# Optimization experiments

Hardware: AMD Instinct MI355X
Metric: run time of the kernel (lower is better)

The kernel has to match this reference:

```python
import jax, jax.numpy as jnp
import numpy as np

N = 50000      # nodes
E = 800000     # edges
IN = 300       # input feature dim (wiki-cs)
H = 5          # attention heads (hardcoded in module)
D = 32         # hidden dim per head
OUT = 10       # output classes (wiki-cs)
NEG = 0.2      # leaky relu negative slope (hardcoded)


def setup_inputs() -> dict:
    key = jax.random.key(0)
    ks = jax.random.split(key, 18)
    def gl(k, shape, fan_in):
        return jax.random.normal(k, shape, jnp.float32) * (1.0 / np.sqrt(fan_in))
    return {
        "features": jax.random.normal(ks[0], (N, IN), jnp.float32),
        "src": jax.random.randint(ks[1], (E,), 0, N, dtype=jnp.int32),
        "dst": jax.random.randint(ks[2], (E,), 0, N, dtype=jnp.int32),
        "W0": gl(ks[3], (IN, H * D), IN),
        "al0": gl(ks[4], (H, D), D),
        "ar0": gl(ks[5], (H, D), D),
        "W1": gl(ks[6], (H * D, H * D), H * D),
        "al1": gl(ks[7], (H, D), D),
        "ar1": gl(ks[8], (H, D), D),
        "W2": gl(ks[9], (H * D, H * D), H * D),
        "al2": gl(ks[10], (H, D), D),
        "ar2": gl(ks[11], (H, D), D),
        "Wout": gl(ks[12], (H * D, OUT), H * D),
        "alout": gl(ks[13], (1, OUT), OUT),
        "arout": gl(ks[14], (1, OUT), OUT),
        "Wraw": gl(ks[15], (IN, H * D), IN),
        "braw": jnp.zeros((H * D,), jnp.float32),
    }


def _gat(x, W, al, ar, src, dst):
    # DGL GATConv: project, per-edge LeakyReLU attention logits,
    # segment-softmax over incoming edges per dst node, weighted scatter-sum.
    Hh, Dd = al.shape
    feat = (x @ W).reshape(N, Hh, Dd)                 # [N,H,D]
    el = jnp.sum(feat * al, axis=-1)                  # [N,H]
    er = jnp.sum(feat * ar, axis=-1)                  # [N,H]
    e = jax.nn.leaky_relu(el[src] + er[dst], NEG)     # [E,H]
    emax = jax.ops.segment_max(e, dst, num_segments=N)
    ew = jnp.exp(e - emax[dst])
    denom = jax.ops.segment_sum(ew, dst, num_segments=N)
    alpha = ew / denom[dst]                           # [E,H]
    msg = feat[src] * alpha[:, :, None]               # [E,H,D]
    return jax.ops.segment_sum(msg, dst, num_segments=N)  # [N,H,D]


def reference(features, src, dst, W0, al0, ar0, W1, al1, ar1, W2, al2, ar2,
              Wout, alout, arout, Wraw, braw):
    # degree-normalized residual aggregation (GResConv with graph_res=raw_res=True)
    deg = jax.ops.segment_sum(jnp.ones((E,), jnp.float32), dst, num_segments=N)
    norm = jnp.maximum(deg, 1.0) ** -0.5              # [N]
    raw = features @ Wraw + braw                      # [N, H*D]
    # input conv: GAT + relu + flatten
    h = jax.nn.relu(_gat(features, W0, al0, ar0, src, dst)).reshape(N, H * D)
    for (W, al, ar) in ((W1, al1, ar1), (W2, al2, ar2)):
        res = raw * norm[:, None]
        res = jax.ops.segment_sum(res[src], dst, num_segments=N) * norm[:, None]
        h = jax.nn.relu(_gat(h, W, al, ar, src, dst).reshape(N, H * D) + res)
    out = _gat(h, Wout, alout, arout, src, dst)       # [N,1,OUT]
    return out.mean(axis=1)                           # [N,OUT]
```

## Files before the change

### kernel.cpp

```cpp
#include <hip/hip_runtime.h>
#include <hip/hip_bf16.h>

#define NEGS 0.2f

typedef __attribute__((ext_vector_type(8))) short bf16x8;
typedef __attribute__((ext_vector_type(4))) float f32x4;

__device__ inline unsigned short bf16_rne(float x) {
    unsigned u = __float_as_uint(x);
    unsigned r = u + 0x7FFFu + ((u >> 16) & 1u);
    return (unsigned short)(r >> 16);
}

__global__ void k_degi(const int* __restrict__ dst, int* __restrict__ deg, int E) {
    int e = blockIdx.x * blockDim.x + threadIdx.x;
    if (e < E) atomicAdd(&deg[dst[e]], 1);
}

__global__ __launch_bounds__(256)
void k_scan1(const int* __restrict__ deg, int* __restrict__ rowptr,
             int* __restrict__ bsum, float* __restrict__ norm, int N) {
    __shared__ int sdata[256];
    int t = threadIdx.x, i = blockIdx.x * 256 + t;
    int d = (i < N) ? deg[i] : 0;
    sdata[t] = d;
    __syncthreads();
    for (int off = 1; off < 256; off <<= 1) {
        int v = (t >= off) ? sdata[t - off] : 0;
        __syncthreads();
        sdata[t] += v;
        __syncthreads();
    }
    if (i < N) {
        rowptr[i] = sdata[t] - d;
        norm[i] = rsqrtf(fmaxf((float)d, 1.0f));
    }
    if (t == 255) bsum[blockIdx.x] = sdata[255];
}

__global__ __launch_bounds__(256)
void k_scan2(const int* __restrict__ bsum, int* __restrict__ boff,
             int* __restrict__ rowptrN, int nb) {
    __shared__ int sdata[256];
    int t = threadIdx.x;
    int v = (t < nb) ? bsum[t] : 0;
    sdata[t] = v;
    __syncthreads();
    for (int off = 1; off < 256; off <<= 1) {
        int x = (t >= off) ? sdata[t - off] : 0;
        __syncthreads();
        sdata[t] += x;
        __syncthreads();
    }
    if (t < nb) boff[t] = sdata[t] - v;
    if (t == 255) *rowptrN = sdata[255];
}

__global__ __launch_bounds__(256)
void k_scan3(int* __restrict__ rowptr, const int* __restrict__ boff, int N) {
    int i = blockIdx.x * 256 + threadIdx.x;
    if (i < N) rowptr[i] += boff[blockIdx.x];
}

__global__ void k_fill(const int* __restrict__ src, const int* __restrict__ dst,
                       const int* __restrict__ rowptr, int* __restrict__ cnt,
                       int* __restrict__ csr_src, int E) {
    int e = blockIdx.x * blockDim.x + threadIdx.x;
    if (e >= E) return;
    int d = dst[e];
    int pos = rowptr[d] + atomicAdd(&cnt[d], 1);
    csr_src[pos] = src[e];
}

__global__ void k_splitX(const float* __restrict__ X, unsigned short* __restrict__ hi,
                         unsigned short* __restrict__ lo, int Nr, int K, int KP) {
    int i = blockIdx.x * blockDim.x + threadIdx.x;
    if (i >= Nr * KP) return;
    int n = i / KP, k = i - n * KP;
    float x = (k < K) ? X[(size_t)n * K + k] : 0.0f;
    unsigned short h = bf16_rne(x);
    float hf = __uint_as_float((unsigned)h << 16);
    hi[i] = h;
    lo[i] = bf16_rne(x - hf);
}

__global__ void k_splitWT(const float* __restrict__ W, unsigned short* __restrict__ hi,
                          unsigned short* __restrict__ lo, int K, int KP) {
    int i = blockIdx.x * blockDim.x + threadIdx.x;
    if (i >= 160 * KP) return;
    int c = i / KP, k = i - c * KP;
    float x = (k < K) ? W[(size_t)k * 160 + c] : 0.0f;
    unsigned short h = bf16_rne(x);
    float hf = __uint_as_float((unsigned)h << 16);
    hi[i] = h;
    lo[i] = bf16_rne(x - hf);
}

template<int NT>
__global__ __launch_bounds__(256)
void k_gemm_mfma(const unsigned short* __restrict__ Xhi, const unsigned short* __restrict__ Xlo,
                 const unsigned short* __restrict__ WThi, const unsigned short* __restrict__ WTlo,
                 const float* __restrict__ bias, const float* __restrict__ rowscale,
                 float* __restrict__ C, int Nrows,
                 const float* __restrict__ al, const float* __restrict__ ar,
                 float* __restrict__ el, float* __restrict__ er) {
    constexpr int KP = NT * 32;
    const int lane = threadIdx.x & 63;
    const int wave = threadIdx.x >> 6;
    const int row0 = blockIdx.x * 64 + wave * 16;
    const int lr = lane & 15;
    const int lq = lane >> 4;

    int arow = row0 + lr;
    int arow_c = (arow < Nrows) ? arow : (Nrows - 1);
    const unsigned short* pah = Xhi + (size_t)arow_c * KP + lq * 8;
    const unsigned short* pal = Xlo + (size_t)arow_c * KP + lq * 8;

    f32x4 acc[10] = {};
    for (int kt = 0; kt < NT; ++kt) {
        bf16x8 ah = *(const bf16x8*)(pah + kt * 32);
        bf16x8 al8 = *(const bf16x8*)(pal + kt * 32);
        #pragma unroll
        for (int ct = 0; ct < 10; ++ct) {
            const unsigned short* pbh = WThi + (size_t)(ct * 16 + lr) * KP + kt * 32 + lq * 8;
            const unsigned short* pbl = WTlo + (size_t)(ct * 16 + lr) * KP + kt * 32 + lq * 8;
            bf16x8 bh = *(const bf16x8*)pbh;
            bf16x8 bl = *(const bf16x8*)pbl;
            acc[ct] = __builtin_amdgcn_mfma_f32_16x16x32_bf16(ah, bh, acc[ct], 0, 0, 0);
            acc[ct] = __builtin_amdgcn_mfma_f32_16x16x32_bf16(ah, bl, acc[ct], 0, 0, 0);
            acc[ct] = __builtin_amdgcn_mfma_f32_16x16x32_bf16(al8, bh, acc[ct], 0, 0, 0);
        }
    }

    #pragma unroll
    for (int i = 0; i < 4; ++i) {
        int row = row0 + lq * 4 + i;
        if (row >= Nrows) continue;
        float sc = rowscale ? rowscale[row] : 1.0f;
        #pragma unroll
        for (int ct = 0; ct < 10; ++ct) {
            int col = ct * 16 + lr;
            float v = acc[ct][i];
            if (bias) v += bias[col];
            C[(size_t)row * 160 + col] = v * sc;
        }
    }

    if (al) {
        float alv0[5], alv1[5], arv0[5], arv1[5];
        #pragma unroll
        for (int h = 0; h < 5; ++h) {
            alv0[h] = al[h * 32 + lr]; alv1[h] = al[h * 32 + 16 + lr];
            arv0[h] = ar[h * 32 + lr]; arv1[h] = ar[h * 32 + 16 + lr];
        }
        #pragma unroll
        for (int i = 0; i < 4; ++i) {
            int row = row0 + lq * 4 + i;
            #pragma unroll
            for (int h = 0; h < 5; ++h) {
                float e_l = acc[2 * h][i] * alv0[h] + acc[2 * h + 1][i] * alv1[h];
                float e_r = acc[2 * h][i] * arv0[h] + acc[2 * h + 1][i] * arv1[h];
                #pragma unroll
                for (int off2 = 8; off2; off2 >>= 1) {
                    e_l += __shfl_xor(e_l, off2, 64);
                    e_r += __shfl_xor(e_r, off2, 64);
                }
                if (lr == h && row < Nrows) {
                    el[row * 5 + h] = e_l;
                    er[row * 5 + h] = e_r;
                }
            }
        }
    }
}

__global__ __launch_bounds__(256)
void k_gemv10(const float* __restrict__ A, const float* __restrict__ B,
              float* __restrict__ C, int Nrows, int K) {
    __shared__ float Bs[160 * 10];
    for (int i = threadIdx.x; i < K * 10; i += 256) Bs[i] = B[i];
    __syncthreads();
    int row = blockIdx.x * 256 + threadIdx.x;
    if (row >= Nrows) return;
    float acc[10] = {};
    const float4* a = reinterpret_cast<const float4*>(A + (size_t)row * K);
    for (int kq = 0; kq < K / 4; ++kq) {
        float4 v = a[kq];
        int k = kq * 4;
        #pragma unroll
        for (int j = 0; j < 10; ++j)
            acc[j] += v.x * Bs[(k + 0) * 10 + j] + v.y * Bs[(k + 1) * 10 + j]
                    + v.z * Bs[(k + 2) * 10 + j] + v.w * Bs[(k + 3) * 10 + j];
    }
    #pragma unroll
    for (int j = 0; j < 10; ++j) C[(size_t)row * 10 + j] = acc[j];
}

__global__ void k_elr_gen(const float* __restrict__ feat, const float* __restrict__ al,
                          const float* __restrict__ ar, float* __restrict__ el,
                          float* __restrict__ er, int N, int H, int D) {
    int i = blockIdx.x * blockDim.x + threadIdx.x;
    if (i >= N * H) return;
    int h = i % H;
    const float* f = feat + (size_t)i * D;
    const float* a = al + h * D;
    const float* b = ar + h * D;
    float sl = 0.0f, sr = 0.0f;
    for (int d = 0; d < D; d++) { float v = f[d]; sl += v * a[d]; sr += v * b[d]; }
    el[i] = sl; er[i] = sr;
}

template<int H, int D>
__global__ __launch_bounds__(64)
void k_gat_fused(const int* __restrict__ rowptr, const int* __restrict__ csr_src,
                 const float* __restrict__ el, const float* __restrict__ er,
                 const float* __restrict__ feat, const float* __restrict__ res,
                 float* __restrict__ out, unsigned short* __restrict__ ohi,
                 unsigned short* __restrict__ olo, int relu_mode) {
    constexpr int HD = H * D;
    const int n = blockIdx.x;
    const int lane = threadIdx.x;
    const int beg = rowptr[n], end = rowptr[n + 1];

    float erh[H];
    #pragma unroll
    for (int h = 0; h < H; ++h) erh[h] = er[n * H + h];

    float m[H], ssum[H];
    #pragma unroll
    for (int h = 0; h < H; ++h) { m[h] = -1e30f; ssum[h] = 0.0f; }
    for (int j = beg + lane; j < end; j += 64) {
        int s = csr_src[j];
        #pragma unroll
        for (int h = 0; h < H; ++h) {
            float x = el[s * H + h] + erh[h];
            x = (x > 0.0f) ? x : (NEGS * x);
            float mn = fmaxf(m[h], x);
            ssum[h] = ssum[h] * __expf(m[h] - mn) + __expf(x - mn);
            m[h] = mn;
        }
    }
    float inv[H];
    #pragma unroll
    for (int h = 0; h < H; ++h) {
        #pragma unroll
        for (int off = 32; off; off >>= 1) {
            float mo = __shfl_xor(m[h], off, 64);
            float so = __shfl_xor(ssum[h], off, 64);
            float mn = fmaxf(m[h], mo);
            ssum[h] = ssum[h] * __expf(m[h] - mn) + so * __expf(mo - mn);
            m[h] = mn;
        }
        inv[h] = (ssum[h] > 0.0f) ? 1.0f / ssum[h] : 0.0f;
    }

    __shared__ float s_alpha[64 * H];
    __shared__ int   s_src[64];

    if constexpr ((D & 3) == 0) {
        constexpr int NV = HD / 4;
        const int hc = (lane * 4) / D;
        float4 acc = make_float4(0.f, 0.f, 0.f, 0.f);
        for (int chunk = beg; chunk < end; chunk += 64) {
            int j = chunk + lane;
            if (j < end) {
                int s = csr_src[j];
                s_src[lane] = s;
                #pragma unroll
                for (int h = 0; h < H; ++h) {
                    float x = el[s * H + h] + erh[h];
                    x = (x > 0.0f) ? x : (NEGS * x);
                    s_alpha[lane * H + h] = __expf(x - m[h]) * inv[h];
                }
            }
            __syncthreads();
            int cnt = min(64, end - chunk);
            if (lane < NV) {
                for (int t = 0; t < cnt; ++t) {
                    const float4 v = *reinterpret_cast<const float4*>(
                        feat + (size_t)s_src[t] * HD + lane * 4);
                    float a = s_alpha[t * H + hc];
                    acc.x += a * v.x; acc.y += a * v.y;
                    acc.z += a * v.z; acc.w += a * v.w;
                }
            }
            __syncthreads();
        }
        if (lane < NV) {
            float4 v = acc;
            if (relu_mode == 2) {
                const float4 rv = *reinterpret_cast<const float4*>(
                    res + (size_t)n * HD + lane * 4);
                v.x += rv.x; v.y += rv.y; v.z += rv.z; v.w += rv.w;
            }
            if (relu_mode) {
                v.x = fmaxf(v.x, 0.f); v.y = fmaxf(v.y, 0.f);
                v.z = fmaxf(v.z, 0.f); v.w = fmaxf(v.w, 0.f);
            }
            *reinterpret_cast<float4*>(out + (size_t)n * HD + lane * 4) = v;
            if (ohi) {
                ushort4 hv, lv;
                float c[4] = {v.x, v.y, v.z, v.w};
                unsigned short hh[4], ll[4];
                #pragma unroll
                for (int e2 = 0; e2 < 4; ++e2) {
                    hh[e2] = bf16_rne(c[e2]);
                    float hf = __uint_as_float((unsigned)hh[e2] << 16);
                    ll[e2] = bf16_rne(c[e2] - hf);
                }
                hv.x = hh[0]; hv.y = hh[1]; hv.z = hh[2]; hv.w = hh[3];
                lv.x = ll[0]; lv.y = ll[1]; lv.z = ll[2]; lv.w = ll[3];
                *reinterpret_cast<ushort4*>(ohi + (size_t)n * HD + lane * 4) = hv;
                *reinterpret_cast<ushort4*>(olo + (size_t)n * HD + lane * 4) = lv;
            }
        }
    } else {
        constexpr int SLOTS = (HD + 63) / 64;
        float acc[SLOTS];
        #pragma unroll
        for (int r = 0; r < SLOTS; ++r) acc[r] = 0.0f;
        for (int chunk = beg; chunk < end; chunk += 64) {
            int j = chunk + lane;
            if (j < end) {
                int s = csr_src[j];
                s_src[lane] = s;
                #pragma unroll
                for (int h = 0; h < H; ++h) {
                    float x = el[s * H + h] + erh[h];
                    x = (x > 0.0f) ? x : (NEGS * x);
                    s_alpha[lane * H + h] = __expf(x - m[h]) * inv[h];
                }
            }
            __syncthreads();
            int cnt = min(64, end - chunk);
            for (int t = 0; t < cnt; ++t) {
                const float* fr = feat + (size_t)s_src[t] * HD;
                #pragma unroll
                for (int r = 0; r < SLOTS; ++r) {
                    int hd = r * 64 + lane;
                    if (hd < HD)
                        acc[r] += s_alpha[t * H + hd / D] * fr[hd];
                }
            }
            __syncthreads();
        }
        #pragma unroll
        for (int r = 0; r < SLOTS; ++r) {
            int hd = r * 64 + lane;
            if (hd < HD) {
                float v = acc[r];
                if (relu_mode == 2) v += res[(size_t)n * HD + hd];
                if (relu_mode) v = fmaxf(v, 0.0f);
                out[(size_t)n * HD + hd] = v;
            }
        }
    }
}

__global__ void k_res_gather4(const int* __restrict__ rowptr, const int* __restrict__ csr_src,
                              const float* __restrict__ rawn, const float* __restrict__ norm,
                              float* __restrict__ res, int N) {
    constexpr int M4 = 40;
    int i = blockIdx.x * blockDim.x + threadIdx.x;
    if (i >= N * M4) return;
    int n = i / M4, q = i - n * M4;
    int beg = rowptr[n], end = rowptr[n + 1];
    float4 acc = make_float4(0.f, 0.f, 0.f, 0.f);
    for (int j = beg; j < end; ++j) {
        const float4 v = *reinterpret_cast<const float4*>(
            rawn + (size_t)csr_src[j] * 160 + q * 4);
        acc.x += v.x; acc.y += v.y; acc.z += v.z; acc.w += v.w;
    }
    float sc = norm[n];
    acc.x *= sc; acc.y *= sc; acc.z *= sc; acc.w *= sc;
    *reinterpret_cast<float4*>(res + (size_t)n * 160 + q * 4) = acc;
}

extern "C" void kernel_launch(void* const* d_in, const int* in_sizes, int n_in,
                              void* d_out, int out_size, void* d_ws, size_t ws_size,
                              hipStream_t stream) {
    const float* features = (const float*)d_in[0];
    const int*   src      = (const int*)d_in[1];
    const int*   dst      = (const int*)d_in[2];
    const float* W0   = (const float*)d_in[3];
    const float* al0  = (const float*)d_in[4];
    const float* ar0  = (const float*)d_in[5];
    const float* W1   = (const float*)d_in[6];
    const float* al1  = (const float*)d_in[7];
    const float* ar1  = (const float*)d_in[8];
    const float* W2   = (const float*)d_in[9];
    const float* al2  = (const float*)d_in[10];
    const float* ar2  = (const float*)d_in[11];
    const float* Wout = (const float*)d_in[12];
    const float* alout= (const float*)d_in[13];
    const float* arout= (const float*)d_in[14];
    const float* Wraw = (const float*)d_in[15];
    const float* braw = (const float*)d_in[16];

    const int IN = 300, INP = 320, H = 5, D = 32, HD = 160, OUT = 10;
    const int N = in_sizes[0] / IN;
    const int E = in_sizes[1];

    char* w = (char*)d_ws;
    auto take = [&](size_t bytes) { char* r = w; w += (bytes + 255) & ~size_t(255); return r; };
    int*   deg     = (int*)  take((size_t)N * 4);
    int*   cnt     = (int*)  take((size_t)N * 4);
    int*   rowptr  = (int*)  take((size_t)(N + 1) * 4);
    int*   csr_src = (int*)  take((size_t)E * 4);
    int*   bsum    = (int*)  take(256 * 4);
    int*   boff    = (int*)  take(256 * 4);
    float* norm    = (float*)take((size_t)N * 4);
    float* el      = (float*)take((size_t)N * H * 4);
    float* er      = (float*)take((size_t)N * H * 4);
    float* res     = (float*)take((size_t)N * HD * 4);
    float* featP   = (float*)take((size_t)N * HD * 4);
    float* hbuf    = (float*)take((size_t)N * HD * 4);
    unsigned short* fhi = (unsigned short*)take((size_t)N * INP * 2);
    unsigned short* flo = (unsigned short*)take((size_t)N * INP * 2);
    unsigned short* wrh = (unsigned short*)take((size_t)160 * INP * 2);
    unsigned short* wrl = (unsigned short*)take((size_t)160 * INP * 2);
    unsigned short* w0h = (unsigned short*)take((size_t)160 * INP * 2);
    unsigned short* w0l = (unsigned short*)take((size_t)160 * INP * 2);
    unsigned short* w1h = (unsigned short*)take((size_t)160 * HD * 2);
    unsigned short* w1l = (unsigned short*)take((size_t)160 * HD * 2);
    unsigned short* w2h = (unsigned short*)take((size_t)160 * HD * 2);
    unsigned short* w2l = (unsigned short*)take((size_t)160 * HD * 2);
    float* out = (float*)d_out;

    unsigned short* hAhi = fhi;
    unsigned short* hAlo = fhi + (size_t)N * HD;
    unsigned short* hBhi = flo;
    unsigned short* hBlo = flo + (size_t)N * HD;

    auto cdiv = [](long long a, long long b) { return (int)((a + b - 1) / b); };
    const int nb = cdiv(N, 256);

    hipMemsetAsync(deg, 0, (size_t)N * 4, stream);
    hipMemsetAsync(cnt, 0, (size_t)N * 4, stream);
    k_degi<<<cdiv(E, 256), 256, 0, stream>>>(dst, deg, E);
    k_scan1<<<nb, 256, 0, stream>>>(deg, rowptr, bsum, norm, N);
    k_scan2<<<1, 256, 0, stream>>>(bsum, boff, rowptr + N, nb);
    k_scan3<<<nb, 256, 0, stream>>>(rowptr, boff, N);
    k_fill<<<cdiv(E, 256), 256, 0, stream>>>(src, dst, rowptr, cnt, csr_src, E);

    k_splitWT<<<cdiv(160 * INP, 256), 256, 0, stream>>>(Wraw, wrh, wrl, IN, INP);
    k_splitWT<<<cdiv(160 * INP, 256), 256, 0, stream>>>(W0, w0h, w0l, IN, INP);
    k_splitWT<<<cdiv(160 * HD, 256), 256, 0, stream>>>(W1, w1h, w1l, HD, HD);
    k_splitWT<<<cdiv(160 * HD, 256), 256, 0, stream>>>(W2, w2h, w2l, HD, HD);
    k_splitX<<<cdiv((long long)N * INP, 256), 256, 0, stream>>>(features, fhi, flo, N, IN, INP);

    k_gemm_mfma<10><<<cdiv(N, 64), 256, 0, stream>>>(fhi, flo, wrh, wrl, braw, norm, featP, N,
                                                     nullptr, nullptr, nullptr, nullptr);

    k_res_gather4<<<cdiv((long long)N * 40, 256), 256, 0, stream>>>(rowptr, csr_src, featP, norm, res, N);

    k_gemm_mfma<10><<<cdiv(N, 64), 256, 0, stream>>>(fhi, flo, w0h, w0l, nullptr, nullptr, featP, N,
                                                     al0, ar0, el, er);
    k_gat_fused<5, 32><<<N, 64, 0, stream>>>(rowptr, csr_src, el, er, featP, nullptr,
                                             hbuf, hAhi, hAlo, 1);

    k_gemm_mfma<5><<<cdiv(N, 64), 256, 0, stream>>>(hAhi, hAlo, w1h, w1l, nullptr, nullptr, featP, N,
                                                    al1, ar1, el, er);
    k_gat_fused<5, 32><<<N, 64, 0, stream>>>(rowptr, csr_src, el, er, featP, res,
                                             hbuf, hBhi, hBlo, 2);

    k_gemm_mfma<5><<<cdiv(N, 64), 256, 0, stream>>>(hBhi, hBlo, w2h, w2l, nullptr, nullptr, featP, N,
                                                    al2, ar2, el, er);
    k_gat_fused<5, 32><<<N, 64, 0, stream>>>(rowptr, csr_src, el, er, featP, res,
                                             hbuf, nullptr, nullptr, 2);

    k_gemv10<<<cdiv(N, 256), 256, 0, stream>>>(hbuf, Wout, featP, N, HD);
    k_elr_gen<<<cdiv(N, 256), 256, 0, stream>>>(featP, alout, arout, el, er, N, 1, OUT);
    k_gat_fused<1, 10><<<N, 64, 0, stream>>>(rowptr, csr_src, el, er, featP, nullptr,
                                             out, nullptr, nullptr, 0);
}
```

Before: 959.1 us.

## Rewrite projection GEMM with 32x32 MFMA and double-buffered LDS weight tiles

Replaces the 16x16x32 MFMA GEMM, which read weight fragments straight from global memory, with a 32x32x16 MFMA kernel. It stages hi/lo weight tiles in double-buffered shared memory and prefetches the next A and B k-slices while computing, and each block now covers 128 rows. The el/er attention-logit epilogue is moved out of the GEMM into a separate vectorized k_elr32 kernel. This adds extra launches and a re-read of the projected features in exchange for better operand reuse and less global weight traffic.

```diff
diff --git a/kernel.cpp b/kernel.cpp
--- a/kernel.cpp
+++ b/kernel.cpp
@@ -5,6 +5,7 @@
 
 typedef __attribute__((ext_vector_type(8))) short bf16x8;
 typedef __attribute__((ext_vector_type(4))) float f32x4;
+typedef __attribute__((ext_vector_type(16))) float f32x16;
 
 __device__ inline unsigned short bf16_rne(float x) {
     unsigned u = __float_as_uint(x);
@@ -96,80 +97,93 @@
     lo[i] = bf16_rne(x - hf);
 }
 
-template<int NT>
+template<int KP>
 __global__ __launch_bounds__(256)
-void k_gemm_mfma(const unsigned short* __restrict__ Xhi, const unsigned short* __restrict__ Xlo,
-                 const unsigned short* __restrict__ WThi, const unsigned short* __restrict__ WTlo,
-                 const float* __restrict__ bias, const float* __restrict__ rowscale,
-                 float* __restrict__ C, int Nrows,
-                 const float* __restrict__ al, const float* __restrict__ ar,
-                 float* __restrict__ el, float* __restrict__ er) {
-    constexpr int KP = NT * 32;
-    const int lane = threadIdx.x & 63;
-    const int wave = threadIdx.x >> 6;
-    const int row0 = blockIdx.x * 64 + wave * 16;
-    const int lr = lane & 15;
-    const int lq = lane >> 4;
-
-    int arow = row0 + lr;
-    int arow_c = (arow < Nrows) ? arow : (Nrows - 1);
-    const unsigned short* pah = Xhi + (size_t)arow_c * KP + lq * 8;
-    const unsigned short* pal = Xlo + (size_t)arow_c * KP + lq * 8;
-
-    f32x4 acc[10] = {};
-    for (int kt = 0; kt < NT; ++kt) {
-        bf16x8 ah = *(const bf16x8*)(pah + kt * 32);
-        bf16x8 al8 = *(const bf16x8*)(pal + kt * 32);
-        #pragma unroll
-        for (int ct = 0; ct < 10; ++ct) {
-            const unsigned short* pbh = WThi + (size_t)(ct * 16 + lr) * KP + kt * 32 + lq * 8;
-            const unsigned short* pbl = WTlo + (size_t)(ct * 16 + lr) * KP + kt * 32 + lq * 8;
-            bf16x8 bh = *(const bf16x8*)pbh;
-            bf16x8 bl = *(const bf16x8*)pbl;
-            acc[ct] = __builtin_amdgcn_mfma_f32_16x16x32_bf16(ah, bh, acc[ct], 0, 0, 0);
-            acc[ct] = __builtin_amdgcn_mfma_f32_16x16x32_bf16(ah, bl, acc[ct], 0, 0, 0);
-            acc[ct] = __builtin_amdgcn_mfma_f32_16x16x32_bf16(al8, bh, acc[ct], 0, 0, 0);
-        }
+void k_gemm_mfma32(const unsigned short* __restrict__ Xhi, const unsigned short* __restrict__ Xlo,
+                   const unsigned short* __restrict__ WThi, const unsigned short* __restrict__ WTlo,
+                   const float* __restrict__ bias, const float* __restrict__ rowscale,
+                   float* __restrict__ C, int Nrows) {
+    constexpr int NKT = KP / 32;
+    __shared__ __align__(16) unsigned short Bs[2][2][160][40];
+    const int tid = threadIdx.x;
+    const int lane = tid & 63;
+    const int wave = tid >> 6;
+    const int lc = lane & 31;
+    const int lh = lane >> 5;
+    const int row0 = blockIdx.x * 128 + wave * 32;
+
+    int arow = row0 + lc;
+    int arc = (arow < Nrows) ? arow : (Nrows - 1);
+    const unsigned short* pAh = Xhi + (size_t)arc * KP + lh * 8;
+    const unsigned short* pAl = Xlo + (size_t)arc * KP + lh * 8;
+
+    bf16x8 breg[5];
+    auto loadB = [&](int kt) {
+        #pragma unroll
+        for (int j = 0; j < 5; ++j) {
+            int idx = tid + j * 256;
+            const unsigned short* sp = (idx < 640) ? WThi : WTlo;
+            int i = (idx < 640) ? idx : idx - 640;
+            int col = i >> 2, ko = (i & 3) * 8;
+            breg[j] = *(const bf16x8*)(sp + (size_t)col * KP + kt * 32 + ko);
+        }
+    };
+    auto storeB = [&](int buf) {
+        #pragma unroll
+        for (int j = 0; j < 5; ++j) {
+            int idx = tid + j * 256;
+            int hl = (idx < 640) ? 0 : 1;
+            int i = idx - hl * 640;
+            int col = i >> 2, ko = (i & 3) * 8;
+            *(bf16x8*)(&Bs[buf][hl][col][ko]) = breg[j];
+        }
+    };
+    bf16x8 Ah[2], Al[2];
+    auto loadA = [&](int kt, bf16x8* ah, bf16x8* al) {
+        #pragma unroll
+        for (int k16 = 0; k16 < 2; ++k16) {
+            ah[k16] = *(const bf16x8*)(pAh + kt * 32 + k16 * 16);
+            al[k16] = *(const bf16x8*)(pAl + kt * 32 + k16 * 16);
+        }
+    };
+
+    f32x16 acc[5] = {};
+    loadB(0); loadA(0, Ah, Al);
+    storeB(0);
+    __syncthreads();
+    for (int kt = 0; kt < NKT; ++kt) {
+        int cur = kt & 1;
+        bf16x8 Ah2[2], Al2[2];
+        if (kt + 1 < NKT) { loadB(kt + 1); loadA(kt + 1, Ah2, Al2); }
+        #pragma unroll
+        for (int k16 = 0; k16 < 2; ++k16) {
+            #pragma unroll
+            for (int ct = 0; ct < 5; ++ct) {
+                bf16x8 bh = *(const bf16x8*)(&Bs[cur][0][ct * 32 + lc][k16 * 16 + lh * 8]);
+                bf16x8 bl = *(const bf16x8*)(&Bs[cur][1][ct * 32 + lc][k16 * 16 + lh * 8]);
+                acc[ct] = __builtin_amdgcn_mfma_f32_32x32x16_bf16(Ah[k16], bh, acc[ct], 0, 0, 0);
+                acc[ct] = __builtin_amdgcn_mfma_f32_32x32x16_bf16(Ah[k16], bl, acc[ct], 0, 0, 0);
+                acc[ct] = __builtin_amdgcn_mfma_f32_32x32x16_bf16(Al[k16], bh, acc[ct], 0, 0, 0);
+            }
+        }
+        if (kt + 1 < NKT) {
+            storeB(cur ^ 1);
+            Ah[0] = Ah2[0]; Ah[1] = Ah2[1]; Al[0] = Al2[0]; Al[1] = Al2[1];
+        }
+        __syncthreads();
     }
 
     #pragma unroll
-    for (int i = 0; i < 4; ++i) {
-        int row = row0 + lq * 4 + i;
+    for (int r = 0; r < 16; ++r) {
+        int row = row0 + (r & 3) + 8 * (r >> 2) + 4 * lh;
         if (row >= Nrows) continue;
         float sc = rowscale ? rowscale[row] : 1.0f;
         #pragma unroll
-        for (int ct = 0; ct < 10; ++ct) {
-            int col = ct * 16 + lr;
-            float v = acc[ct][i];
+        for (int ct = 0; ct < 5; ++ct) {
+            int col = ct * 32 + lc;
+            float v = acc[ct][r];
             if (bias) v += bias[col];
             C[(size_t)row * 160 + col] = v * sc;
-        }
-    }
-
-    if (al) {
-        float alv0[5], alv1[5], arv0[5], arv1[5];
-        #pragma unroll
-        for (int h = 0; h < 5; ++h) {
-            alv0[h] = al[h * 32 + lr]; alv1[h] = al[h * 32 + 16 + lr];
-            arv0[h] = ar[h * 32 + lr]; arv1[h] = ar[h * 32 + 16 + lr];
-        }
-        #pragma unroll
-        for (int i = 0; i < 4; ++i) {
-            int row = row0 + lq * 4 + i;
-            #pragma unroll
-            for (int h = 0; h < 5; ++h) {
-                float e_l = acc[2 * h][i] * alv0[h] + acc[2 * h + 1][i] * alv1[h];
-                float e_r = acc[2 * h][i] * arv0[h] + acc[2 * h + 1][i] * arv1[h];
-                #pragma unroll
-                for (int off2 = 8; off2; off2 >>= 1) {
-                    e_l += __shfl_xor(e_l, off2, 64);
-                    e_r += __shfl_xor(e_r, off2, 64);
-                }
-                if (lr == h && row < Nrows) {
-                    el[row * 5 + h] = e_l;
-                    er[row * 5 + h] = e_r;
-                }
-            }
         }
     }
 }
@@ -194,6 +208,25 @@
     }
     #pragma unroll
     for (int j = 0; j < 10; ++j) C[(size_t)row * 10 + j] = acc[j];
+}
+
+__global__ void k_elr32(const float* __restrict__ feat, const float* __restrict__ al,
+                        const float* __restrict__ ar, float* __restrict__ el,
+                        float* __restrict__ er, int N, int H) {
+    int i = blockIdx.x * blockDim.x + threadIdx.x;
+    if (i >= N * H) return;
+    int h = i % H;
+    const float4* f = (const float4*)(feat + (size_t)i * 32);
+    const float4* a = (const float4*)(al + h * 32);
+    const float4* b = (const float4*)(ar + h * 32);
+    float sl = 0.0f, sr = 0.0f;
+    #pragma unroll
+    for (int d = 0; d < 8; d++) {
+        float4 v = f[d], x = a[d], y = b[d];
+        sl += v.x * x.x + v.y * x.y + v.z * x.z + v.w * x.w;
+        sr += v.x * y.x + v.y * y.y + v.z * y.z + v.w * y.w;
+    }
+    el[i] = sl; er[i] = sr;
 }
 
 __global__ void k_elr_gen(const float* __restrict__ feat, const float* __restrict__ al,
@@ -449,23 +482,22 @@
     k_splitWT<<<cdiv(160 * HD, 256), 256, 0, stream>>>(W2, w2h, w2l, HD, HD);
     k_splitX<<<cdiv((long long)N * INP, 256), 256, 0, stream>>>(features, fhi, flo, N, IN, INP);
 
-    k_gemm_mfma<10><<<cdiv(N, 64), 256, 0, stream>>>(fhi, flo, wrh, wrl, braw, norm, featP, N,
-                                                     nullptr, nullptr, nullptr, nullptr);
+    k_gemm_mfma32<320><<<cdiv(N, 128), 256, 0, stream>>>(fhi, flo, wrh, wrl, braw, norm, featP, N);
 
     k_res_gather4<<<cdiv((long long)N * 40, 256), 256, 0, stream>>>(rowptr, csr_src, featP, norm, res, N);
 
-    k_gemm_mfma<10><<<cdiv(N, 64), 256, 0, stream>>>(fhi, flo, w0h, w0l, nullptr, nullptr, featP, N,
-                                                     al0, ar0, el, er);
+    k_gemm_mfma32<320><<<cdiv(N, 128), 256, 0, stream>>>(fhi, flo, w0h, w0l, nullptr, nullptr, featP, N);
+    k_elr32<<<cdiv((long long)N * H, 256), 256, 0, stream>>>(featP, al0, ar0, el, er, N, H);
     k_gat_fused<5, 32><<<N, 64, 0, stream>>>(rowptr, csr_src, el, er, featP, nullptr,
                                              hbuf, hAhi, hAlo, 1);
 
-    k_gemm_mfma<5><<<cdiv(N, 64), 256, 0, stream>>>(hAhi, hAlo, w1h, w1l, nullptr, nullptr, featP, N,
-                                                    al1, ar1, el, er);
+    k_gemm_mfma32<160><<<cdiv(N, 128), 256, 0, stream>>>(hAhi, hAlo, w1h, w1l, nullptr, nullptr, featP, N);
+    k_elr32<<<cdiv((long long)N * H, 256), 256, 0, stream>>>(featP, al1, ar1, el, er, N, H);
     k_gat_fused<5, 32><<<N, 64, 0, stream>>>(rowptr, csr_src, el, er, featP, res,
                                              hbuf, hBhi, hBlo, 2);
 
-    k_gemm_mfma<5><<<cdiv(N, 64), 256, 0, stream>>>(hBhi, hBlo, w2h, w2l, nullptr, nullptr, featP, N,
-                                                    al2, ar2, el, er);
+    k_gemm_mfma32<160><<<cdiv(N, 128), 256, 0, stream>>>(hBhi, hBlo, w2h, w2l, nullptr, nullptr, featP, N);
+    k_elr32<<<cdiv((long long)N * H, 256), 256, 0, stream>>>(featP, al2, ar2, el, er, N, H);
     k_gat_fused<5, 32><<<N, 64, 0, stream>>>(rowptr, csr_src, el, er, featP, res,
                                              hbuf, nullptr, nullptr, 2);
 
```

Measured after the change: 779.2 us. 18.8% less time.
